# Performance work log

Hardware: AMD Instinct MI355X
Metric: run time of the kernel (lower is better)

## Reference

```python
import jax, jax.numpy as jnp
import numpy as np

B, S, H, NH = 4, 1024, 3072, 32
D = H // NH  # head_dim = 96
I = 8192
EPS = 1e-5


def _layernorm(x, g, b):
    mu = jnp.mean(x, axis=-1, keepdims=True)
    var = jnp.mean(jnp.square(x - mu), axis=-1, keepdims=True)
    return (x - mu) * jax.lax.rsqrt(var + EPS) * g + b


def _gelu_tanh(x):
    c = np.sqrt(2.0 / np.pi).astype(np.float32)
    return 0.5 * x * (1.0 + jnp.tanh(c * (x + 0.044715 * x * x * x)))


def setup_inputs() -> dict:
    key = jax.random.key(0)
    ks = jax.random.split(key, 8)
    s = 0.02
    causal = jnp.tril(jnp.ones((S, S), dtype=bool))[None, None]  # [1,1,S,S]
    return {
        "hidden_states": jax.random.normal(ks[0], (B, S, H), jnp.float32),
        "attention_mask": causal,
        "Wq": jax.random.normal(ks[1], (H, H), jnp.float32) * s,
        "Wk": jax.random.normal(ks[2], (H, H), jnp.float32) * s,
        "Wv": jax.random.normal(ks[3], (H, H), jnp.float32) * s,
        "Wo": jax.random.normal(ks[4], (H, H), jnp.float32) * s,
        "bo": jnp.zeros((H,), jnp.float32),
        "ln1_g": jnp.ones((H,), jnp.float32),
        "ln1_b": jnp.zeros((H,), jnp.float32),
        "ln2_g": jnp.ones((H,), jnp.float32),
        "ln2_b": jnp.zeros((H,), jnp.float32),
        "W1": jax.random.normal(ks[5], (H, I), jnp.float32) * s,
        "b1": jnp.zeros((I,), jnp.float32),
        "W2": jax.random.normal(ks[6], (I, H), jnp.float32) * s,
        "b2": jnp.zeros((H,), jnp.float32),
    }


def reference(hidden_states, attention_mask, Wq, Wk, Wv, Wo, bo,
              ln1_g, ln1_b, ln2_g, ln2_b, W1, b1, W2, b2):
    x = hidden_states
    # --- pre-attention LN ---
    h = _layernorm(x, ln1_g, ln1_b)
    # --- attention ---
    q = (h @ Wq).reshape(B, S, NH, D).transpose(0, 2, 1, 3)  # [B,NH,S,D]
    k = (h @ Wk).reshape(B, S, NH, D).transpose(0, 2, 1, 3)
    v = (h @ Wv).reshape(B, S, NH, D).transpose(0, 2, 1, 3)
    scale = 1.0 / np.sqrt(D).astype(np.float32)
    scores = jnp.einsum("bhqd,bhkd->bhqk", q, k) * scale  # [B,NH,S,S]
    scores = jnp.where(attention_mask, scores, jnp.float32(-1e9))
    probs = jax.nn.softmax(scores, axis=-1)
    ctx = jnp.einsum("bhqk,bhkd->bhqd", probs, v)  # [B,NH,S,D]
    ctx = ctx.transpose(0, 2, 1, 3).reshape(B, S, H)
    attn_out = ctx @ Wo + bo
    x = x + attn_out
    # --- MLP ---
    h = _layernorm(x, ln2_g, ln2_b)
    mlp = _gelu_tanh(h @ W1 + b1) @ W2 + b2
    return x + mlp
```

## Files before the change

### kernel.cpp

```cpp
#include <hip/hip_runtime.h>
#include <hip/hip_bf16.h>

typedef __attribute__((ext_vector_type(8))) short short8;
typedef __attribute__((ext_vector_type(4))) float f32x4;
typedef __hip_bfloat16 bf16;

#define GLDS16(gp, lp) __builtin_amdgcn_global_load_lds( \
    (const __attribute__((address_space(1))) void*)(gp), \
    (__attribute__((address_space(3))) void*)(lp), 16, 0, 0)

__device__ __forceinline__ short f2bf(float f){
  bf16 h = __float2bfloat16(f);
  return *reinterpret_cast<short*>(&h);
}

__global__ __launch_bounds__(256) void wconv_kernel(
    const float* __restrict__ W, bf16* __restrict__ Wt, int K, int N)
{
  __shared__ float tile[32][33];
  const int tk = blockIdx.y * 32, tn = blockIdx.x * 32;
  const int t = threadIdx.x;
#pragma unroll
  for (int i = 0; i < 4; ++i){
    int idx = i*256 + t, r = idx >> 5, c = idx & 31;
    tile[r][c] = W[(size_t)(tk + r) * N + (tn + c)];
  }
  __syncthreads();
#pragma unroll
  for (int i = 0; i < 4; ++i){
    int idx = i*256 + t, r = idx >> 5, c = idx & 31;
    Wt[(size_t)(tn + r) * K + (tk + c)] = __float2bfloat16(tile[c][r]);
  }
}

__global__ __launch_bounds__(256) void ln_kernel(
    const float* __restrict__ x, const float* __restrict__ g,
    const float* __restrict__ bb, bf16* __restrict__ out)
{
  const int row = blockIdx.x, t = threadIdx.x;
  const float4* xr = (const float4*)(x + (size_t)row * 3072);
  float4 v[3];
  float s = 0.f, s2 = 0.f;
#pragma unroll
  for (int i = 0; i < 3; ++i){
    v[i] = xr[i*256 + t];
    s  += v[i].x + v[i].y + v[i].z + v[i].w;
    s2 += v[i].x*v[i].x + v[i].y*v[i].y + v[i].z*v[i].z + v[i].w*v[i].w;
  }
#pragma unroll
  for (int d = 1; d < 64; d <<= 1){ s += __shfl_xor(s, d); s2 += __shfl_xor(s2, d); }
  __shared__ float red[2][4];
  const int w = t >> 6, lane = t & 63;
  if (lane == 0){ red[0][w] = s; red[1][w] = s2; }
  __syncthreads();
  s  = red[0][0] + red[0][1] + red[0][2] + red[0][3];
  s2 = red[1][0] + red[1][1] + red[1][2] + red[1][3];
  const float mu = s * (1.f/3072.f);
  const float rstd = rsqrtf(s2 * (1.f/3072.f) - mu*mu + 1e-5f);
  const float4* g4 = (const float4*)g;
  const float4* b4 = (const float4*)bb;
  uint2* ov = (uint2*)(out + (size_t)row * 3072);
#pragma unroll
  for (int i = 0; i < 3; ++i){
    const int c = i*256 + t;
    float4 gv = g4[c], bv = b4[c], xv = v[i];
    float o0 = (xv.x - mu) * rstd * gv.x + bv.x;
    float o1 = (xv.y - mu) * rstd * gv.y + bv.y;
    float o2 = (xv.z - mu) * rstd * gv.z + bv.z;
    float o3 = (xv.w - mu) * rstd * gv.w + bv.w;
    uint2 pk;
    pk.x = (unsigned)(unsigned short)f2bf(o0) | ((unsigned)(unsigned short)f2bf(o1) << 16);
    pk.y = (unsigned)(unsigned short)f2bf(o2) | ((unsigned)(unsigned short)f2bf(o3) << 16);
    ov[c] = pk;
  }
}

template<int EPI>
__global__ __launch_bounds__(512, 2) void gemm8_kernel(
    const bf16* __restrict__ A, const bf16* __restrict__ Bt,
    const float* __restrict__ bias, const float* __restrict__ res,
    void* __restrict__ outp, int M, int N, int K)
{
  __shared__ __align__(16) char lds[131072];
  const int NT = K >> 5;
  const int nbx = N >> 8;
  const int nwg = nbx * (M >> 8);
  const int cpx = nwg >> 3;
  const int bid = blockIdx.x;
  const int lg = (bid & 7) * cpx + (bid >> 3);
  const int by = lg / nbx, bx = lg - by * nbx;
  const int m0 = by << 8, n0 = bx << 8;

  const int tid = threadIdx.x;
  const int lane = tid & 63, wid = tid >> 6;
  const int wm = wid >> 2, wn = wid & 3;
  const int l15 = lane & 15, lhi = lane >> 4;

  const int row0 = tid >> 2;
  const int ce = ((tid & 3) ^ ((tid >> 3) & 3)) * 8;
  const bf16* pA0 = A  + (size_t)(m0 + row0) * K + ce;
  const bf16* pA1 = pA0 + (size_t)128 * K;
  const bf16* pB0 = Bt + (size_t)(n0 + row0) * K + ce;
  const bf16* pB1 = pB0 + (size_t)128 * K;

  auto stageA = [&](int u){
    if (u < NT){
      char* d = lds + ((u & 3) << 15) + (tid << 4);
      GLDS16(pA0 + ((size_t)u << 5), d);
      GLDS16(pA1 + ((size_t)u << 5), d + 8192);
    }
  };
  auto stageB = [&](int u){
    if (u < NT){
      char* d = lds + ((u & 3) << 15) + 16384 + (tid << 4);
      GLDS16(pB0 + ((size_t)u << 5), d);
      GLDS16(pB1 + ((size_t)u << 5), d + 8192);
    }
  };

  f32x4 acc[8][4];
#pragma unroll
  for (int i = 0; i < 8; ++i)
#pragma unroll
    for (int j = 0; j < 4; ++j) acc[i][j] = (f32x4){0.f,0.f,0.f,0.f};

  const int swz = (lhi ^ ((l15 >> 1) & 3)) << 4;
  const int aoff = (wm*128 + l15)*64 + swz;
  const int boff = 16384 + (wn*64 + l15)*64 + swz;

  stageA(0); stageB(0); stageA(1); stageB(1); stageA(2); stageB(2);

  for (int t = 0; t < NT; ++t){
    const char* Lb = lds + ((t & 3) << 15);
    asm volatile("s_waitcnt vmcnt(8)" ::: "memory");
    __builtin_amdgcn_s_barrier();
    __builtin_amdgcn_sched_barrier(0);

    stageA(t + 3);
    short8 a[4], b[4];
#pragma unroll
    for (int i = 0; i < 4; ++i) a[i] = *(const short8*)(Lb + aoff + i*1024);
#pragma unroll
    for (int i = 0; i < 4; ++i) b[i] = *(const short8*)(Lb + boff + i*1024);
    __builtin_amdgcn_s_setprio(1);
#pragma unroll
    for (int mi = 0; mi < 4; ++mi)
#pragma unroll
      for (int ni = 0; ni < 4; ++ni)
        acc[mi][ni] = __builtin_amdgcn_mfma_f32_16x16x32_bf16(a[mi], b[ni], acc[mi][ni], 0,0,0);
    __builtin_amdgcn_s_setprio(0);

    stageB(t + 3);
#pragma unroll
    for (int i = 0; i < 4; ++i) a[i] = *(const short8*)(Lb + aoff + (4+i)*1024);
    __builtin_amdgcn_s_setprio(1);
#pragma unroll
    for (int mi = 0; mi < 4; ++mi)
#pragma unroll
      for (int ni = 0; ni < 4; ++ni)
        acc[4+mi][ni] = __builtin_amdgcn_mfma_f32_16x16x32_bf16(a[mi], b[ni], acc[4+mi][ni], 0,0,0);
    __builtin_amdgcn_s_setprio(0);
  }

  const int rb = m0 + wm*128 + (lhi << 2);
  const int cb0 = n0 + wn*64 + l15;
#pragma unroll
  for (int mi = 0; mi < 8; ++mi){
#pragma unroll
    for (int ni = 0; ni < 4; ++ni){
      const int col = cb0 + ni*16;
#pragma unroll
      for (int r = 0; r < 4; ++r){
        const int row = rb + mi*16 + r;
        float vv = acc[mi][ni][r];
        if constexpr (EPI == 0){
          const int cbuf = col / 3072;
          const int cl = col - cbuf*3072;
          ((bf16*)outp)[(size_t)cbuf*M*3072 + (size_t)row*3072 + cl] = __float2bfloat16(vv);
        } else if constexpr (EPI == 1){
          ((float*)outp)[(size_t)row*N + col] = vv + bias[col] + res[(size_t)row*N + col];
        } else {
          float xx = vv + bias[col];
          float y = 0.7978845608f*(xx + 0.044715f*xx*xx*xx);
          float e = exp2f(fminf(y, 15.f) * 2.885390082f);
          ((bf16*)outp)[(size_t)row*N + col] = __float2bfloat16(xx * e / (e + 1.f));
        }
      }
    }
  }
}

__global__ __launch_bounds__(256) void vt_kernel(
    const bf16* __restrict__ V, bf16* __restrict__ VT)
{
  const int bh = blockIdx.x, st = blockIdx.y;
  const int b = bh >> 5, h = bh & 31;
  const int t = threadIdx.x;
  __shared__ __align__(16) short tile[96][72];
  const int s0 = st*64;
  const short* src = (const short*)V + (size_t)(b*1024 + s0)*3072 + h*96;
#pragma unroll
  for (int i = 0; i < 3; ++i){
    int c = t + i*256;
    int s = c/12, dc = c - s*12;
    short8 v8 = *(const short8*)(src + (size_t)s*3072 + dc*8);
#pragma unroll
    for (int e = 0; e < 8; ++e) tile[dc*8+e][s] = v8[e];
  }
  __syncthreads();
  short* dst = (short*)VT + ((size_t)bh*96)*1024 + s0;
#pragma unroll
  for (int i = 0; i < 3; ++i){
    int c = t + i*256;
    int d = c >> 3, kc = c & 7;
    short8 v8 = *(const short8*)(&tile[0][0] + d*72 + kc*8);
    *(short8*)(dst + (size_t)d*1024 + kc*8) = v8;
  }
}

__global__ __launch_bounds__(256, 4) void attn_kernel(
    const bf16* __restrict__ Q, const bf16* __restrict__ Kg,
    const bf16* __restrict__ VT, bf16* __restrict__ O)
{
  const int bh = blockIdx.x;
  const int yp = blockIdx.y;
  const int b = bh >> 5, h = bh & 31;
  const int t = threadIdx.x;
  const int lane = t & 63, w = t >> 6;
  const size_t RS = 3072;
  const size_t base = (size_t)(b * 1024) * RS + (size_t)h * 96;
  const short* VTh = (const short*)VT + (size_t)bh * 96 * 1024;

  __shared__ __align__(16) bf16 Ks[64*128];
  __shared__ __align__(16) bf16 Vt[96*64];
  __shared__ __align__(16) bf16 Ps[4][16][72];

  char* KsB = (char*)Ks;
  char* VtB = (char*)Vt;
  const short* PsW = (const short*)&Ps[w][0][0];
  const float sc = 0.1020620726f * 1.44269504089f;
  const int l15 = lane & 15, lhi = lane >> 4;

#pragma unroll
  for (int sel = 0; sel < 2; ++sel){
    const int qt = sel ? (15 - yp) : yp;
    const int q0 = qt*64 + w*16;

    short8 aq[3];
    {
      const short* qp = (const short*)Q + base + (size_t)(q0 + l15) * RS + (lhi << 3);
#pragma unroll
      for (int ks = 0; ks < 3; ++ks) aq[ks] = *(const short8*)(qp + ks*32);
    }
    f32x4 acc[6];
#pragma unroll
    for (int i = 0; i < 6; ++i) acc[i] = (f32x4){0.f,0.f,0.f,0.f};
    float mrow[4] = {-3e38f,-3e38f,-3e38f,-3e38f};
    float lrow[4] = {0.f,0.f,0.f,0.f};

    for (int kt = 0; kt <= qt; ++kt){
      const int kv0 = kt*64;
      __syncthreads();
      {
        short8 kr[4], vr[3];
#pragma unroll
        for (int i = 0; i < 4; ++i){
          int c = t + i*256, kv = c >> 4, dc = c & 15;
          kr[i] = *(const short8*)((const short*)Kg + base + (size_t)(kv0 + kv)*RS + dc*8);
        }
#pragma unroll
        for (int i = 0; i < 3; ++i){
          int c = t + i*256, d = c >> 3, kvc = c & 7;
          vr[i] = *(const short8*)(VTh + (size_t)d*1024 + kv0 + kvc*8);
        }
#pragma unroll
        for (int i = 0; i < 4; ++i){
          int c = t + i*256, kv = c >> 4, dc = c & 15;
          *(short8*)(KsB + kv*256 + ((dc ^ (kv & 7)) << 4)) = kr[i];
        }
#pragma unroll
        for (int i = 0; i < 3; ++i){
          int c = t + i*256, d = c >> 3, kvc = c & 7;
          *(short8*)(VtB + d*128 + ((kvc ^ (d & 7)) << 4)) = vr[i];
        }
      }
      __syncthreads();

      float sv[4][4];
      const bool diag = (kt == qt);
#pragma unroll
      for (int ct = 0; ct < 4; ++ct){
        const int kvl = ct*16 + l15;
        f32x4 s4 = (f32x4){0.f,0.f,0.f,0.f};
#pragma unroll
        for (int ks = 0; ks < 3; ++ks){
          short8 bk = *(const short8*)(KsB + kvl*256 + (((ks*4 + lhi) ^ (kvl & 7)) << 4));
          s4 = __builtin_amdgcn_mfma_f32_16x16x32_bf16(aq[ks], bk, s4, 0,0,0);
        }
#pragma unroll
        for (int r = 0; r < 4; ++r){
          float vvl = s4[r] * sc;
          if (diag){
            int kvg = kv0 + kvl;
            int qg  = q0 + (lhi << 2) + r;
            if (kvg > qg) vvl = -3e38f;
          }
          sv[ct][r] = vvl;
        }
      }

      float alpha[4];
#pragma unroll
      for (int r = 0; r < 4; ++r){
        float m = fmaxf(fmaxf(sv[0][r], sv[1][r]), fmaxf(sv[2][r], sv[3][r]));
#pragma unroll
        for (int dd = 1; dd < 16; dd <<= 1) m = fmaxf(m, __shfl_xor(m, dd));
        float mn = fmaxf(mrow[r], m);
        alpha[r] = exp2f(mrow[r] - mn);
        mrow[r] = mn;
        float rs = 0.f;
#pragma unroll
        for (int ct = 0; ct < 4; ++ct){
          float p = exp2f(sv[ct][r] - mn);
          sv[ct][r] = p;
          rs += p;
        }
#pragma unroll
        for (int dd = 1; dd < 16; dd <<= 1) rs += __shfl_xor(rs, dd);
        lrow[r] = lrow[r]*alpha[r] + rs;
      }
#pragma unroll
      for (int i = 0; i < 6; ++i)
#pragma unroll
        for (int r = 0; r < 4; ++r) acc[i][r] *= alpha[r];

#pragma unroll
      for (int ct = 0; ct < 4; ++ct)
#pragma unroll
        for (int r = 0; r < 4; ++r)
          Ps[w][(lhi << 2) + r][ct*16 + l15] = __float2bfloat16(sv[ct][r]);

#pragma unroll
      for (int ks2 = 0; ks2 < 2; ++ks2){
        short8 pa = *(const short8*)(PsW + l15*72 + ks2*32 + (lhi << 3));
#pragma unroll
        for (int dt = 0; dt < 6; ++dt){
          const int dl = dt*16 + l15;
          short8 vbf = *(const short8*)(VtB + dl*128 + (((ks2*4 + lhi) ^ (dl & 7)) << 4));
          acc[dt] = __builtin_amdgcn_mfma_f32_16x16x32_bf16(pa, vbf, acc[dt], 0,0,0);
        }
      }
    }

    bf16* Ob = (bf16*)O + base + (size_t)q0 * RS;
#pragma unroll
    for (int dt = 0; dt < 6; ++dt){
#pragma unroll
      for (int r = 0; r < 4; ++r){
        float vvl = acc[dt][r] / lrow[r];
        Ob[(size_t)((lhi << 2) + r) * RS + dt*16 + l15] = __float2bfloat16(vvl);
      }
    }
  }
}

extern "C" void kernel_launch(void* const* d_in, const int* in_sizes, int n_in,
                              void* d_out, int out_size, void* d_ws, size_t ws_size,
                              hipStream_t stream)
{
  (void)in_sizes; (void)n_in; (void)out_size; (void)ws_size;
  const float* x_in = (const float*)d_in[0];
  const float* Wq   = (const float*)d_in[2];
  const float* Wk   = (const float*)d_in[3];
  const float* Wv   = (const float*)d_in[4];
  const float* Wo   = (const float*)d_in[5];
  const float* bo   = (const float*)d_in[6];
  const float* ln1g = (const float*)d_in[7];
  const float* ln1b = (const float*)d_in[8];
  const float* ln2g = (const float*)d_in[9];
  const float* ln2b = (const float*)d_in[10];
  const float* W1   = (const float*)d_in[11];
  const float* b1   = (const float*)d_in[12];
  const float* W2   = (const float*)d_in[13];
  const float* b2   = (const float*)d_in[14];

  char* ws = (char*)d_ws;
  size_t off = 0;
  auto alloc = [&](size_t bytes) -> char* {
    char* p = ws + off; off += (bytes + 255) & ~(size_t)255; return p;
  };
  const size_t H = 3072, I = 8192, M = 4096;
  bf16* Wqt = (bf16*)alloc(H*H*2);
  bf16* Wkt = (bf16*)alloc(H*H*2);
  bf16* Wvt = (bf16*)alloc(H*H*2);
  bf16* Wot = (bf16*)alloc(H*H*2);
  bf16* W1t = (bf16*)alloc(H*I*2);
  bf16* W2t = (bf16*)alloc(H*I*2);
  bf16* hb  = (bf16*)alloc(M*H*2);
  bf16* qb  = (bf16*)alloc(M*H*2);
  bf16* kb  = (bf16*)alloc(M*H*2);
  bf16* vb  = (bf16*)alloc(M*H*2);
  bf16* ctx = (bf16*)alloc(M*H*2);
  float* x2 = (float*)d_out;
  bf16* h2  = hb;
  bf16* VT  = hb;
  bf16* act = qb;
  (void)kb; (void)vb;

  wconv_kernel<<<dim3(96, 96),  256, 0, stream>>>(Wq, Wqt, 3072, 3072);
  wconv_kernel<<<dim3(96, 96),  256, 0, stream>>>(Wk, Wkt, 3072, 3072);
  wconv_kernel<<<dim3(96, 96),  256, 0, stream>>>(Wv, Wvt, 3072, 3072);
  wconv_kernel<<<dim3(96, 96),  256, 0, stream>>>(Wo, Wot, 3072, 3072);
  wconv_kernel<<<dim3(256, 96), 256, 0, stream>>>(W1, W1t, 3072, 8192);
  wconv_kernel<<<dim3(96, 256), 256, 0, stream>>>(W2, W2t, 8192, 3072);

  ln_kernel<<<4096, 256, 0, stream>>>(x_in, ln1g, ln1b, hb);

  gemm8_kernel<0><<<576, 512, 0, stream>>>(hb, Wqt, nullptr, nullptr, qb, 4096, 9216, 3072);

  vt_kernel<<<dim3(128, 16), 256, 0, stream>>>(vb, VT);

  attn_kernel<<<dim3(128, 8), 256, 0, stream>>>(qb, kb, VT, ctx);

  gemm8_kernel<1><<<192, 512, 0, stream>>>(ctx, Wot, bo, x_in, x2, 4096, 3072, 3072);

  ln_kernel<<<4096, 256, 0, stream>>>(x2, ln2g, ln2b, h2);

  gemm8_kernel<2><<<512, 512, 0, stream>>>(h2, W1t, b1, nullptr, act, 4096, 8192, 3072);

  gemm8_kernel<1><<<192, 512, 0, stream>>>(act, W2t, b2, x2, (float*)d_out, 4096, 3072, 8192);
}
```

Measured before the change: 1.025 ms.

## Rework GEMM mainloop to 32x32x16 MFMA with BK=64 double-buffered phases

Replaces the 16x16x32 MFMA tiling with 32x32x16 MFMA on a K-tile of 64, double-buffered in LDS with a new XOR swizzle. Each K-tile is split into four phases that interleave LDS fragment reads, async global-to-LDS staging of the next tile, and MFMA bursts, separated by barriers. The larger MFMA shape is meant to cut LDS read traffic and instruction count per FLOP. In exchange, prefetch depth drops from three stages to one, and the added barriers per phase could expose memory latency.

```diff
diff --git a/kernel.cpp b/kernel.cpp
--- a/kernel.cpp
+++ b/kernel.cpp
@@ -3,6 +3,7 @@
 
 typedef __attribute__((ext_vector_type(8))) short short8;
 typedef __attribute__((ext_vector_type(4))) float f32x4;
+typedef __attribute__((ext_vector_type(16))) float f32x16;
 typedef __hip_bfloat16 bf16;
 
 #define GLDS16(gp, lp) __builtin_amdgcn_global_load_lds( \
@@ -82,7 +83,7 @@
     void* __restrict__ outp, int M, int N, int K)
 {
   __shared__ __align__(16) char lds[131072];
-  const int NT = K >> 5;
+  const int NT = K >> 6;
   const int nbx = N >> 8;
   const int nwg = nbx * (M >> 8);
   const int cpx = nwg >> 3;
@@ -94,85 +95,93 @@
   const int tid = threadIdx.x;
   const int lane = tid & 63, wid = tid >> 6;
   const int wm = wid >> 2, wn = wid & 3;
-  const int l15 = lane & 15, lhi = lane >> 4;
-
-  const int row0 = tid >> 2;
-  const int ce = ((tid & 3) ^ ((tid >> 3) & 3)) * 8;
-  const bf16* pA0 = A  + (size_t)(m0 + row0) * K + ce;
-  const bf16* pA1 = pA0 + (size_t)128 * K;
-  const bf16* pB0 = Bt + (size_t)(n0 + row0) * K + ce;
-  const bf16* pB1 = pB0 + (size_t)128 * K;
-
-  auto stageA = [&](int u){
+  const int l31 = lane & 31, l32 = lane >> 5;
+
+  const int srow = tid >> 3;
+  const int ce = ((tid & 7) ^ (srow & 7)) * 8;
+  const bf16* pA = A  + (size_t)(m0 + srow) * K + ce;
+  const bf16* pB = Bt + (size_t)(n0 + srow) * K + ce;
+
+  auto stageA = [&](int u, int h){
     if (u < NT){
-      char* d = lds + ((u & 3) << 15) + (tid << 4);
-      GLDS16(pA0 + ((size_t)u << 5), d);
-      GLDS16(pA1 + ((size_t)u << 5), d + 8192);
+      char* d = lds + ((u & 1) << 16) + (h << 14) + (tid << 4);
+      const bf16* g0 = pA + (size_t)(h * 128) * K + ((size_t)u << 6);
+      GLDS16(g0, d);
+      GLDS16(g0 + (size_t)64 * K, d + 8192);
     }
   };
-  auto stageB = [&](int u){
+  auto stageB = [&](int u, int h){
     if (u < NT){
-      char* d = lds + ((u & 3) << 15) + 16384 + (tid << 4);
-      GLDS16(pB0 + ((size_t)u << 5), d);
-      GLDS16(pB1 + ((size_t)u << 5), d + 8192);
+      char* d = lds + ((u & 1) << 16) + 32768 + (h << 14) + (tid << 4);
+      const bf16* g0 = pB + (size_t)(h * 128) * K + ((size_t)u << 6);
+      GLDS16(g0, d);
+      GLDS16(g0 + (size_t)64 * K, d + 8192);
     }
   };
 
-  f32x4 acc[8][4];
-#pragma unroll
-  for (int i = 0; i < 8; ++i)
-#pragma unroll
-    for (int j = 0; j < 4; ++j) acc[i][j] = (f32x4){0.f,0.f,0.f,0.f};
-
-  const int swz = (lhi ^ ((l15 >> 1) & 3)) << 4;
-  const int aoff = (wm*128 + l15)*64 + swz;
-  const int boff = 16384 + (wn*64 + l15)*64 + swz;
-
-  stageA(0); stageB(0); stageA(1); stageB(1); stageA(2); stageB(2);
+  f32x16 acc[4][2];
+#pragma unroll
+  for (int i = 0; i < 4; ++i)
+#pragma unroll
+    for (int j = 0; j < 2; ++j)
+#pragma unroll
+      for (int e = 0; e < 16; ++e) acc[i][j][e] = 0.f;
+
+  const int c0 = (l32 ^ (l31 & 1)) << 4;
+  const int sx = (l31 >> 1) & 3;
+  const int arow = wm*16384 + l31*128 + c0;
+  const int brow = 32768 + wn*8192 + l31*128 + c0;
+
+  stageA(0, 0); stageA(0, 1); stageB(0, 0); stageB(0, 1);
+  asm volatile("s_waitcnt vmcnt(0)" ::: "memory");
+  __builtin_amdgcn_s_barrier();
 
   for (int t = 0; t < NT; ++t){
-    const char* Lb = lds + ((t & 3) << 15);
-    asm volatile("s_waitcnt vmcnt(8)" ::: "memory");
-    __builtin_amdgcn_s_barrier();
-    __builtin_amdgcn_sched_barrier(0);
-
-    stageA(t + 3);
-    short8 a[4], b[4];
-#pragma unroll
-    for (int i = 0; i < 4; ++i) a[i] = *(const short8*)(Lb + aoff + i*1024);
-#pragma unroll
-    for (int i = 0; i < 4; ++i) b[i] = *(const short8*)(Lb + boff + i*1024);
-    __builtin_amdgcn_s_setprio(1);
-#pragma unroll
-    for (int mi = 0; mi < 4; ++mi)
-#pragma unroll
-      for (int ni = 0; ni < 4; ++ni)
-        acc[mi][ni] = __builtin_amdgcn_mfma_f32_16x16x32_bf16(a[mi], b[ni], acc[mi][ni], 0,0,0);
-    __builtin_amdgcn_s_setprio(0);
-
-    stageB(t + 3);
-#pragma unroll
-    for (int i = 0; i < 4; ++i) a[i] = *(const short8*)(Lb + aoff + (4+i)*1024);
-    __builtin_amdgcn_s_setprio(1);
-#pragma unroll
-    for (int mi = 0; mi < 4; ++mi)
-#pragma unroll
-      for (int ni = 0; ni < 4; ++ni)
-        acc[4+mi][ni] = __builtin_amdgcn_mfma_f32_16x16x32_bf16(a[mi], b[ni], acc[4+mi][ni], 0,0,0);
-    __builtin_amdgcn_s_setprio(0);
-  }
-
-  const int rb = m0 + wm*128 + (lhi << 2);
-  const int cb0 = n0 + wn*64 + l15;
-#pragma unroll
-  for (int mi = 0; mi < 8; ++mi){
-#pragma unroll
-    for (int ni = 0; ni < 4; ++ni){
-      const int col = cb0 + ni*16;
-#pragma unroll
-      for (int r = 0; r < 4; ++r){
-        const int row = rb + mi*16 + r;
-        float vv = acc[mi][ni][r];
+    const int bufo = (t & 1) << 16;
+    short8 af[4], bf2[2];
+
+#define PHASE(S, STAGES, VM)                                                  \
+    {                                                                         \
+      const int so = ((S ^ sx) << 5) + bufo;                                  \
+      _Pragma("unroll")                                                       \
+      for (int mi = 0; mi < 4; ++mi)                                          \
+        af[mi] = *(const short8*)(lds + so + arow + mi*4096);                 \
+      _Pragma("unroll")                                                       \
+      for (int nj = 0; nj < 2; ++nj)                                          \
+        bf2[nj] = *(const short8*)(lds + so + brow + nj*4096);                \
+      STAGES;                                                                 \
+      __builtin_amdgcn_sched_barrier(0);                                      \
+      __builtin_amdgcn_s_barrier();                                           \
+      __builtin_amdgcn_s_setprio(1);                                          \
+      _Pragma("unroll")                                                       \
+      for (int mi = 0; mi < 4; ++mi)                                          \
+        _Pragma("unroll")                                                     \
+        for (int nj = 0; nj < 2; ++nj)                                        \
+          acc[mi][nj] = __builtin_amdgcn_mfma_f32_32x32x16_bf16(              \
+              af[mi], bf2[nj], acc[mi][nj], 0, 0, 0);                         \
+      __builtin_amdgcn_s_setprio(0);                                          \
+      VM;                                                                     \
+      __builtin_amdgcn_s_barrier();                                           \
+    }
+
+    PHASE(0, stageA(t+1, 0), )
+    PHASE(1, stageA(t+1, 1), )
+    PHASE(2, { stageB(t+1, 0); stageB(t+1, 1); }, )
+    PHASE(3, , asm volatile("s_waitcnt vmcnt(0)" ::: "memory"))
+#undef PHASE
+  }
+
+  const int rb = m0 + wm*128 + 4*l32;
+  const int cb0 = n0 + wn*64 + l31;
+#pragma unroll
+  for (int mi = 0; mi < 4; ++mi){
+#pragma unroll
+    for (int nj = 0; nj < 2; ++nj){
+      const int col = cb0 + nj*32;
+#pragma unroll
+      for (int r = 0; r < 16; ++r){
+        const int row = rb + mi*32 + (r & 3) + 8*(r >> 2);
+        float vv = acc[mi][nj][r];
         if constexpr (EPI == 0){
           const int cbuf = col / 3072;
           const int cl = col - cbuf*3072;
```

Result: slower. 1.118 ms (+9.1%).

## Restructure GEMM LDS pipeline to prefetch depth two with split barriers

Applied to the files above, without the earlier changes.

Reworks the GEMM main loop's global-to-LDS staging. Prefetch depth drops from three tiles ahead to two, and loads are split into four quarter-stages interleaved with the LDS fragment reads. Extra barriers and lgkmcnt waits are added so each half of the MFMA work runs after its fragments have landed, with a vmcnt wait at the end of each iteration. The aim is a finer-grained schedule in the style of ping-pong kernels that overlaps memory with MFMA more evenly, at the cost of more barriers per iteration and a shallower prefetch.

```diff
diff --git a/kernel.cpp b/kernel.cpp
--- a/kernel.cpp
+++ b/kernel.cpp
@@ -103,18 +103,11 @@
   const bf16* pB0 = Bt + (size_t)(n0 + row0) * K + ce;
   const bf16* pB1 = pB0 + (size_t)128 * K;
 
-  auto stageA = [&](int u){
+  auto stage = [&](int u, int j){
     if (u < NT){
-      char* d = lds + ((u & 3) << 15) + (tid << 4);
-      GLDS16(pA0 + ((size_t)u << 5), d);
-      GLDS16(pA1 + ((size_t)u << 5), d + 8192);
-    }
-  };
-  auto stageB = [&](int u){
-    if (u < NT){
-      char* d = lds + ((u & 3) << 15) + 16384 + (tid << 4);
-      GLDS16(pB0 + ((size_t)u << 5), d);
-      GLDS16(pB1 + ((size_t)u << 5), d + 8192);
+      char* d = lds + ((u & 3) << 15) + (j << 13) + (tid << 4);
+      const bf16* g = (j == 0) ? pA0 : (j == 1) ? pA1 : (j == 2) ? pB0 : pB1;
+      GLDS16(g + ((size_t)u << 5), d);
     }
   };
 
@@ -128,20 +121,24 @@
   const int aoff = (wm*128 + l15)*64 + swz;
   const int boff = 16384 + (wn*64 + l15)*64 + swz;
 
-  stageA(0); stageB(0); stageA(1); stageB(1); stageA(2); stageB(2);
+  stage(0,0); stage(0,1); stage(0,2); stage(0,3);
+  stage(1,0); stage(1,1); stage(1,2); stage(1,3);
+  asm volatile("s_waitcnt vmcnt(4)" ::: "memory");
+  __builtin_amdgcn_s_barrier();
 
   for (int t = 0; t < NT; ++t){
     const char* Lb = lds + ((t & 3) << 15);
-    asm volatile("s_waitcnt vmcnt(8)" ::: "memory");
+    short8 a[4], b[4];
+
+#pragma unroll
+    for (int i = 0; i < 4; ++i) a[i] = *(const short8*)(Lb + aoff + i*1024);
+#pragma unroll
+    for (int i = 0; i < 4; ++i) b[i] = *(const short8*)(Lb + boff + i*1024);
+    stage(t + 2, 0); stage(t + 2, 1);
+    __builtin_amdgcn_sched_barrier(0);
     __builtin_amdgcn_s_barrier();
+    asm volatile("s_waitcnt lgkmcnt(0)" ::: "memory");
     __builtin_amdgcn_sched_barrier(0);
-
-    stageA(t + 3);
-    short8 a[4], b[4];
-#pragma unroll
-    for (int i = 0; i < 4; ++i) a[i] = *(const short8*)(Lb + aoff + i*1024);
-#pragma unroll
-    for (int i = 0; i < 4; ++i) b[i] = *(const short8*)(Lb + boff + i*1024);
     __builtin_amdgcn_s_setprio(1);
 #pragma unroll
     for (int mi = 0; mi < 4; ++mi)
@@ -149,10 +146,15 @@
       for (int ni = 0; ni < 4; ++ni)
         acc[mi][ni] = __builtin_amdgcn_mfma_f32_16x16x32_bf16(a[mi], b[ni], acc[mi][ni], 0,0,0);
     __builtin_amdgcn_s_setprio(0);
-
-    stageB(t + 3);
+    __builtin_amdgcn_s_barrier();
+
 #pragma unroll
     for (int i = 0; i < 4; ++i) a[i] = *(const short8*)(Lb + aoff + (4+i)*1024);
+    stage(t + 2, 2); stage(t + 2, 3);
+    __builtin_amdgcn_sched_barrier(0);
+    __builtin_amdgcn_s_barrier();
+    asm volatile("s_waitcnt lgkmcnt(0)" ::: "memory");
+    __builtin_amdgcn_sched_barrier(0);
     __builtin_amdgcn_s_setprio(1);
 #pragma unroll
     for (int mi = 0; mi < 4; ++mi)
@@ -160,6 +162,9 @@
       for (int ni = 0; ni < 4; ++ni)
         acc[4+mi][ni] = __builtin_amdgcn_mfma_f32_16x16x32_bf16(a[mi], b[ni], acc[4+mi][ni], 0,0,0);
     __builtin_amdgcn_s_setprio(0);
+    if (t + 2 < NT) { asm volatile("s_waitcnt vmcnt(4)" ::: "memory"); }
+    else            { asm volatile("s_waitcnt vmcnt(0)" ::: "memory"); }
+    __builtin_amdgcn_s_barrier();
   }
 
   const int rb = m0 + wm*128 + (lhi << 2);
```

New measurement: 1.057 ms. +3.1%, slower.
